# Performance work log

Measured on AMD Instinct MI355X. Metric: run time of the kernel, lower is better.

Reference implementation:

```python
import jax, jax.numpy as jnp
import numpy as np


def setup_inputs() -> dict:
    key = jax.random.key(0)
    k1, k2, k3, k4 = jax.random.split(key, 4)
    B, S, IN, OUT = 4, 2048, 4096, 16384
    x = jax.random.normal(k1, (B, S, IN), dtype=jnp.float32)
    # int8 quantized weights in [-127, 127]; stored as int8
    q_weight = jax.random.randint(k2, (OUT, IN), -127, 128, dtype=jnp.int32).astype(jnp.int8)
    scale = jax.random.uniform(k3, (1,), dtype=jnp.float32, minval=0.005, maxval=0.02)
    bias = jax.random.normal(k4, (OUT,), dtype=jnp.float32)
    return {"x": x, "q_weight": q_weight, "scale": scale, "bias": bias}


def reference(x, q_weight, scale, bias):
    # dequantize: int8 -> fp32, per-tensor scale, then cast to activation dtype
    w = (q_weight.astype(jnp.float32) * scale).astype(x.dtype)  # [OUT, IN]
    # F.linear: y = x @ w.T + bias
    return jnp.einsum('bsi,oi->bso', x, w) + bias.astype(x.dtype)
```

## Files before the change

kernel.cpp:

```cpp
#include <hip/hip_runtime.h>
#include <hip/hip_bf16.h>
#include <stdint.h>


typedef __attribute__((ext_vector_type(4))) float f32x4;
typedef __attribute__((ext_vector_type(4))) int i32x4;
typedef __attribute__((ext_vector_type(8))) short bf16x8s;
typedef __attribute__((ext_vector_type(4))) unsigned int u32x4;

__device__ __forceinline__ uint32_t f2bf_rne(float f) {
  uint32_t x = __float_as_uint(f);
  return (x + 0x7FFFu + ((x >> 16) & 1u)) >> 16;
}
__device__ __forceinline__ uint32_t pk2_rne(float lo, float hi) {
  return f2bf_rne(lo) | (f2bf_rne(hi) << 16);
}
__device__ __forceinline__ uint32_t pk2_trunc(float lo, float hi) {
  return (__float_as_uint(lo) >> 16) | (__float_as_uint(hi) & 0xFFFF0000u);
}

#define GLOAD_LDS16(g, l)                                        \
  __builtin_amdgcn_global_load_lds(                              \
      (const __attribute__((address_space(1))) void*)(g),        \
      (__attribute__((address_space(3))) void*)(l), 16, 0, 0)

__global__ __launch_bounds__(256) void quant_x_kernel(
    const float* __restrict__ x, int8_t* __restrict__ xq,
    float* __restrict__ rscale) {
  const int r = blockIdx.x;
  const int t = threadIdx.x;
  const f32x4* rp = (const f32x4*)(x + (size_t)r * 4096);
  f32x4 v[4];
#pragma unroll
  for (int j = 0; j < 4; ++j)
    v[j] = __builtin_nontemporal_load(rp + t + 256 * j);
  float m = 0.f;
#pragma unroll
  for (int j = 0; j < 4; ++j) {
    m = fmaxf(m, fabsf(v[j].x));
    m = fmaxf(m, fabsf(v[j].y));
    m = fmaxf(m, fabsf(v[j].z));
    m = fmaxf(m, fabsf(v[j].w));
  }
#pragma unroll
  for (int off = 32; off >= 1; off >>= 1)
    m = fmaxf(m, __shfl_xor(m, off, 64));
  __shared__ float wm[4];
  if ((t & 63) == 0) wm[t >> 6] = m;
  __syncthreads();
  float mm = fmaxf(fmaxf(wm[0], wm[1]), fmaxf(wm[2], wm[3]));
  mm = fmaxf(mm, 1e-20f);
  const float inv = 127.0f / mm;
  if (t == 0) rscale[r] = mm * (1.0f / 127.0f);
  uint32_t* orow = (uint32_t*)(xq + (size_t)r * 4096);
#pragma unroll
  for (int j = 0; j < 4; ++j) {
    int q0 = (int)rintf(v[j].x * inv);
    int q1 = (int)rintf(v[j].y * inv);
    int q2 = (int)rintf(v[j].z * inv);
    int q3 = (int)rintf(v[j].w * inv);
    q0 = max(-127, min(127, q0)); q1 = max(-127, min(127, q1));
    q2 = max(-127, min(127, q2)); q3 = max(-127, min(127, q3));
    uint32_t o = (uint32_t)(q0 & 0xFF) | ((uint32_t)(q1 & 0xFF) << 8) |
                 ((uint32_t)(q2 & 0xFF) << 16) | ((uint32_t)(q3 & 0xFF) << 24);
    orow[t + 256 * j] = o;
  }
}

__global__ __launch_bounds__(256) void conv_w_q_kernel(
    const int32_t* __restrict__ w, int8_t* __restrict__ wq, int n16) {
  const int stride = blockDim.x * gridDim.x;
  for (int i = blockIdx.x * blockDim.x + threadIdx.x; i < n16; i += stride) {
    u32x4 o;
#pragma unroll
    for (int j = 0; j < 4; ++j) {
      i32x4 a = __builtin_nontemporal_load((const i32x4*)w + i * 4 + j);
      uint32_t p = (uint32_t)(a.x & 0xFF) | ((uint32_t)(a.y & 0xFF) << 8) |
                   ((uint32_t)(a.z & 0xFF) << 16) |
                   ((uint32_t)(a.w & 0xFF) << 24);
      if (j == 0) o.x = p; else if (j == 1) o.y = p;
      else if (j == 2) o.z = p; else o.w = p;
    }
    ((u32x4*)wq)[i] = o;
  }
}


#define PIN() __builtin_amdgcn_sched_barrier(0)

#define BARRIER()                 \
  PIN();                          \
  __builtin_amdgcn_s_barrier();   \
  PIN()

#define WAIT4  asm volatile("s_waitcnt vmcnt(4)" ::: "memory"); PIN()
#define WAIT0  asm volatile("s_waitcnt vmcnt(0)" ::: "memory"); PIN()
#define WAITL0 asm volatile("s_waitcnt lgkmcnt(0)" ::: "memory"); PIN()
#define LG(N)  asm volatile("s_waitcnt lgkmcnt(" #N ")" ::: "memory"); PIN()

#define STAGE(mat_base, koffb, ldsbase)                                      \
  {                                                                          \
    GLOAD_LDS16((mat_base) + (size_t)srow * RSB + (koffb) + skch,            \
                (ldsbase) + tid * 16);                                       \
    GLOAD_LDS16((mat_base) + (size_t)(srow + 128) * RSB + (koffb) + skch,    \
                (ldsbase) + 8192 + tid * 16);                                \
  }

#define ABLK(buf, kk) ((buf) + (kk) * 16384)
#define BBLK(buf, kk) ((buf) + 32768 + (kk) * 16384)

#define DSR(dst, addr, OFF)                                                  \
  asm volatile("ds_read_b128 %0, %1 offset:" OFF : "=v"(dst) : "v"(addr))

#define READ12(da, db, blkoff)                                               \
  {                                                                          \
    uint32_t _aa = aoff + (blkoff), _bb = boff + (blkoff);                   \
    DSR(db[0], _bb, "0");    DSR(db[1], _bb, "1024");                        \
    DSR(db[2], _bb, "2048"); DSR(db[3], _bb, "3072");                        \
    DSR(da[0], _aa, "0");    DSR(da[1], _aa, "1024");                        \
    DSR(da[2], _aa, "2048"); DSR(da[3], _aa, "3072");                        \
    DSR(da[4], _aa, "4096"); DSR(da[5], _aa, "5120");                        \
    DSR(da[6], _aa, "6144"); DSR(da[7], _aa, "7168");                        \
  }

#define MFMA4(av, bv, j)                                                     \
  _Pragma("unroll") for (int ni = 0; ni < 4; ++ni)                           \
    acc[j][ni] = __builtin_amdgcn_mfma_i32_16x16x64_i8(                      \
        av[j], bv[ni], acc[j][ni], 0, 0, 0);

#define EPOCH_ILV(av, bv, xa, xb, blkoff)                                    \
  {                                                                          \
    uint32_t _aa = aoff + (blkoff), _bb = boff + (blkoff);                   \
    __builtin_amdgcn_s_setprio(1);                                           \
    DSR(xb[0], _bb, "0");    DSR(xb[1], _bb, "1024");   PIN();               \
    LG(9);  MFMA4(av, bv, 0);                           PIN();               \
    DSR(xb[2], _bb, "2048"); DSR(xb[3], _bb, "3072");   PIN();               \
    LG(10); MFMA4(av, bv, 1);                           PIN();               \
    DSR(xa[0], _aa, "0");    DSR(xa[1], _aa, "1024");   PIN();               \
    LG(11); MFMA4(av, bv, 2);                           PIN();               \
    DSR(xa[2], _aa, "2048"); DSR(xa[3], _aa, "3072");   PIN();               \
    LG(12); MFMA4(av, bv, 3);                           PIN();               \
    DSR(xa[4], _aa, "4096"); DSR(xa[5], _aa, "5120");   PIN();               \
    LG(13); MFMA4(av, bv, 4);                           PIN();               \
    DSR(xa[6], _aa, "6144"); DSR(xa[7], _aa, "7168");   PIN();               \
    LG(14); MFMA4(av, bv, 5);                           PIN();               \
    LG(13); MFMA4(av, bv, 6);                           PIN();               \
    LG(12); MFMA4(av, bv, 7);                                                \
    __builtin_amdgcn_s_setprio(0);                                           \
  }

#define MFMA32(av, bv)                                                       \
  __builtin_amdgcn_s_setprio(1);                                             \
  _Pragma("unroll") for (int j = 0; j < 8; ++j)                              \
    _Pragma("unroll") for (int ni = 0; ni < 4; ++ni)                         \
      acc[j][ni] = __builtin_amdgcn_mfma_i32_16x16x64_i8(                    \
          av[j], bv[ni], acc[j][ni], 0, 0, 0);                               \
  __builtin_amdgcn_s_setprio(0);

__global__ __launch_bounds__(512, 2) void qlinear_gemm_i8_kernel(
    const int8_t* __restrict__ Xq,
    const int8_t* __restrict__ Wq,
    const float* __restrict__ rscale,
    const float* __restrict__ scalep,
    const float* __restrict__ bias,
    float* __restrict__ Y)
{
  constexpr int N = 16384, K = 4096;
  constexpr int RSB = K;
  constexpr int NT = K / 128;

  extern __shared__ __align__(16) char lds[];

  const int tid  = threadIdx.x;
  const int lane = tid & 63;
  const int wid  = tid >> 6;
  const int wm   = wid >> 2;
  const int wn   = wid & 3;
  const int r16  = lane & 15;
  const int g4   = lane >> 4;
  const int chb  = (g4 ^ ((r16 >> 1) & 3)) << 4;

  const int srow = tid >> 2;
  const int skch = ((tid & 3) ^ ((tid >> 3) & 3)) * 16;

  const int bid = blockIdx.x;
  const int xcd = bid & 7;
  const int l   = bid >> 3;
  const int bm  = (xcd & 1) * 16 + (l >> 4);
  const int bn  = (xcd >> 1) * 16 + (l & 15);

  i32x4 acc[8][4];
#pragma unroll
  for (int i = 0; i < 8; ++i)
#pragma unroll
    for (int j = 0; j < 4; ++j) acc[i][j] = (i32x4)0;

  i32x4 pa[8], qa[8], pb[4], qb[4];

  const char* Xp = (const char*)Xq + (size_t)(bm * 256) * RSB;
  const char* Wp = (const char*)Wq + (size_t)(bn * 256) * RSB;

  const uint32_t ldsb = (uint32_t)(uintptr_t)(void*)lds;
  const uint32_t aoff = ldsb + (uint32_t)((wm * 128 + r16) * 64 + chb);
  const uint32_t boff = ldsb + (uint32_t)(32768 + (wn * 64 + r16) * 64 + chb);

  STAGE(Xp, 0,   ABLK(lds, 0));
  STAGE(Wp, 0,   BBLK(lds, 0));
  STAGE(Xp, 64,  ABLK(lds, 1));
  STAGE(Wp, 64,  BBLK(lds, 1));
  STAGE(Xp, 128, ABLK(lds + 65536, 0));
  STAGE(Wp, 128, BBLK(lds + 65536, 0));
  WAIT4;
  BARRIER();
  READ12(pa, pb, 0u);

  for (int t = 0; t <= NT - 3; ++t) {
    const uint32_t cur = (uint32_t)(t & 1) << 16;
    const uint32_t nxt = cur ^ 65536u;
    char* cb = lds + cur;
    char* nb = lds + nxt;
    const size_t k1n = (size_t)(t + 1) * 128;
    const size_t k2n = (size_t)(t + 2) * 128;
    STAGE(Xp, k1n + 64, ABLK(nb, 1));
    STAGE(Wp, k1n + 64, BBLK(nb, 1));
    EPOCH_ILV(pa, pb, qa, qb, cur + 16384u);
    WAIT4;
    BARRIER();
    STAGE(Xp, k2n, ABLK(cb, 0));
    STAGE(Wp, k2n, BBLK(cb, 0));
    EPOCH_ILV(qa, qb, pa, pb, nxt);
    WAIT4;
    BARRIER();
  }

  {
    const uint32_t cur = (uint32_t)((NT - 2) & 1) << 16;
    const uint32_t nxt = cur ^ 65536u;
    char* nb = lds + nxt;
    const size_t k1n = (size_t)(NT - 1) * 128;
    STAGE(Xp, k1n + 64, ABLK(nb, 1));
    STAGE(Wp, k1n + 64, BBLK(nb, 1));
    EPOCH_ILV(pa, pb, qa, qb, cur + 16384u);
    WAIT4;
    BARRIER();
    EPOCH_ILV(qa, qb, pa, pb, nxt);
    WAIT0;
    BARRIER();
    EPOCH_ILV(pa, pb, qa, qb, nxt + 16384u);
    WAITL0;
    MFMA32(qa, qb);
  }

  const float s = scalep[0];
  float bv[4];
#pragma unroll
  for (int ni = 0; ni < 4; ++ni)
    bv[ni] = bias[bn * 256 + wn * 64 + ni * 16 + r16];

#pragma unroll
  for (int mi = 0; mi < 8; ++mi) {
    const int grow0 = bm * 256 + wm * 128 + mi * 16 + g4 * 4;
#pragma unroll
    for (int r = 0; r < 4; ++r) {
      const float dr = s * rscale[grow0 + r];
      float* yp = Y + (size_t)(grow0 + r) * N + bn * 256 + wn * 64 + r16;
#pragma unroll
      for (int ni = 0; ni < 4; ++ni)
        yp[ni * 16] = (float)acc[mi][ni][r] * dr + bv[ni];
    }
  }
}

#define BM 128
#define BN 128
#define BK 64
#define LDKF (BK * 2)

__global__ __launch_bounds__(256, 2) void qlinear_fused_kernel(
    const float* __restrict__ X, const int32_t* __restrict__ W,
    const float* __restrict__ scalep, const float* __restrict__ bias,
    float* __restrict__ Y)
{
  constexpr int N = 16384, K = 4096;
  __shared__ __align__(16) char slds[(BM + BN) * LDKF];
  char* As = slds;
  char* Bs = slds + BM * LDKF;
  const int tid = threadIdx.x, lane = tid & 63, wid = tid >> 6;
  const int wr = wid >> 1, wc = wid & 1;
  const int nwg = gridDim.x, cpx = nwg >> 3, bid = blockIdx.x;
  const int swz = (bid & 7) * cpx + (bid >> 3);
  const int ntn = N / BN, bm = swz / ntn, bn = swz % ntn;
  const int r16 = lane & 15, g4 = lane >> 4;
  f32x4 acc[4][4];
#pragma unroll
  for (int i = 0; i < 4; ++i)
#pragma unroll
    for (int j = 0; j < 4; ++j) acc[i][j] = (f32x4)0.f;
  const float* Abase = X + (size_t)(bm * BM) * K;
  const int32_t* Bbase = W + (size_t)(bn * BN) * K;
  const int stg_col = (tid & 7) * 8;
  for (int kt = 0; kt < K / BK; ++kt) {
    const int kb = kt * BK;
    if (kt) __syncthreads();
#pragma unroll
    for (int i = 0; i < 4; ++i) {
      const int row = i * 32 + (tid >> 3);
      const float* p = Abase + (size_t)row * K + kb + stg_col;
      f32x4 v0 = *(const f32x4*)p;
      f32x4 v1 = *(const f32x4*)(p + 4);
      u32x4 o = {pk2_rne(v0.x, v0.y), pk2_rne(v0.z, v0.w),
                 pk2_rne(v1.x, v1.y), pk2_rne(v1.z, v1.w)};
      int byte = (row * LDKF + stg_col * 2) ^ ((row & 7) << 4);
      *(u32x4*)(As + byte) = o;
    }
#pragma unroll
    for (int i = 0; i < 4; ++i) {
      const int row = i * 32 + (tid >> 3);
      const int32_t* p = Bbase + (size_t)row * K + kb + stg_col;
      i32x4 v0 = *(const i32x4*)p;
      i32x4 v1 = *(const i32x4*)(p + 4);
      u32x4 o = {pk2_trunc((float)v0.x, (float)v0.y),
                 pk2_trunc((float)v0.z, (float)v0.w),
                 pk2_trunc((float)v1.x, (float)v1.y),
                 pk2_trunc((float)v1.z, (float)v1.w)};
      int byte = (row * LDKF + stg_col * 2) ^ ((row & 7) << 4);
      *(u32x4*)(Bs + byte) = o;
    }
    __syncthreads();
#pragma unroll
    for (int kk = 0; kk < 2; ++kk) {
      bf16x8s af[4], bfr[4];
#pragma unroll
      for (int mi = 0; mi < 4; ++mi) {
        const int row = wr * 64 + mi * 16 + r16;
        int byte = (row * LDKF + kk * 64 + g4 * 16) ^ ((row & 7) << 4);
        af[mi] = *(const bf16x8s*)(As + byte);
      }
#pragma unroll
      for (int ni = 0; ni < 4; ++ni) {
        const int row = wc * 64 + ni * 16 + r16;
        int byte = (row * LDKF + kk * 64 + g4 * 16) ^ ((row & 7) << 4);
        bfr[ni] = *(const bf16x8s*)(Bs + byte);
      }
#pragma unroll
      for (int mi = 0; mi < 4; ++mi)
#pragma unroll
        for (int ni = 0; ni < 4; ++ni)
          acc[mi][ni] = __builtin_amdgcn_mfma_f32_16x16x32_bf16(
              af[mi], bfr[ni], acc[mi][ni], 0, 0, 0);
    }
  }
  const float s = scalep[0];
  float bv[4];
#pragma unroll
  for (int ni = 0; ni < 4; ++ni)
    bv[ni] = bias[bn * BN + wc * 64 + ni * 16 + r16];
#pragma unroll
  for (int mi = 0; mi < 4; ++mi) {
    const int grow0 = bm * BM + wr * 64 + mi * 16 + g4 * 4;
#pragma unroll
    for (int r = 0; r < 4; ++r) {
      float* yp = Y + (size_t)(grow0 + r) * N + bn * BN + wc * 64 + r16;
#pragma unroll
      for (int ni = 0; ni < 4; ++ni)
        yp[ni * 16] = s * acc[mi][ni][r] + bv[ni];
    }
  }
}

extern "C" void kernel_launch(void* const* d_in, const int* in_sizes, int n_in,
                              void* d_out, int out_size, void* d_ws, size_t ws_size,
                              hipStream_t stream) {
  const float*   x  = (const float*)d_in[0];
  const int32_t* w  = (const int32_t*)d_in[1];
  const float*   sc = (const float*)d_in[2];
  const float*   bs = (const float*)d_in[3];
  float*         y  = (float*)d_out;

  constexpr size_t M = 8192, N = 16384, K = 4096;
  const size_t wq_bytes = N * K;
  const size_t xq_bytes = M * K;
  const size_t need = wq_bytes + xq_bytes + M * sizeof(float);

  if (ws_size >= need) {
    int8_t* wq = (int8_t*)d_ws;
    int8_t* xq = wq + wq_bytes;
    float*  rs = (float*)(xq + xq_bytes);
    hipFuncSetAttribute((const void*)qlinear_gemm_i8_kernel,
                        hipFuncAttributeMaxDynamicSharedMemorySize, 131072);
    quant_x_kernel<<<8192, 256, 0, stream>>>(x, xq, rs);
    conv_w_q_kernel<<<2048, 256, 0, stream>>>(w, wq, (int)(wq_bytes / 16));
    qlinear_gemm_i8_kernel<<<2048, 512, 131072, stream>>>(xq, wq, rs, sc, bs, y);
  } else {
    qlinear_fused_kernel<<<8192, 256, 0, stream>>>(x, w, sc, bs, y);
  }
}
```

Before: 615.4 us.

## Shrink int8 GEMM tile to 128x256 with 4 waves and simple double buffering

The int8 GEMM kernel moves from a 256x256 block tile with 8 waves and a deep interleaved prefetch pipeline to a 128x256 tile with 4 waves. It now uses a single K=64 step per iteration with a two-buffer LDS ping-pong of 48 KB, and launches twice as many blocks. The aims are lower LDS use and higher occupancy, plus simpler scheduling. In exchange it loses the register-level double buffering of LDS reads and waits for all outstanding global loads every iteration. The smaller M tile also lowers arithmetic intensity per byte loaded.

```diff
diff --git a/kernel.cpp b/kernel.cpp
--- a/kernel.cpp
+++ b/kernel.cpp
@@ -93,71 +93,63 @@
   __builtin_amdgcn_s_barrier();   \
   PIN()
 
-#define WAIT4  asm volatile("s_waitcnt vmcnt(4)" ::: "memory"); PIN()
-#define WAIT0  asm volatile("s_waitcnt vmcnt(0)" ::: "memory"); PIN()
-#define WAITL0 asm volatile("s_waitcnt lgkmcnt(0)" ::: "memory"); PIN()
-#define LG(N)  asm volatile("s_waitcnt lgkmcnt(" #N ")" ::: "memory"); PIN()
-
-#define STAGE(mat_base, koffb, ldsbase)                                      \
+#define WAIT0vm asm volatile("s_waitcnt vmcnt(0)" ::: "memory"); PIN()
+#define LG(N)   asm volatile("s_waitcnt lgkmcnt(" #N ")" ::: "memory"); PIN()
+
+#define STAGE_A(mat_base, koffb, ldsbase)                                    \
   {                                                                          \
     GLOAD_LDS16((mat_base) + (size_t)srow * RSB + (koffb) + skch,            \
                 (ldsbase) + tid * 16);                                       \
+    GLOAD_LDS16((mat_base) + (size_t)(srow + 64) * RSB + (koffb) + skch,     \
+                (ldsbase) + 4096 + tid * 16);                                \
+  }
+#define STAGE_B(mat_base, koffb, ldsbase)                                    \
+  {                                                                          \
+    GLOAD_LDS16((mat_base) + (size_t)srow * RSB + (koffb) + skch,            \
+                (ldsbase) + tid * 16);                                       \
+    GLOAD_LDS16((mat_base) + (size_t)(srow + 64) * RSB + (koffb) + skch,     \
+                (ldsbase) + 4096 + tid * 16);                                \
     GLOAD_LDS16((mat_base) + (size_t)(srow + 128) * RSB + (koffb) + skch,    \
                 (ldsbase) + 8192 + tid * 16);                                \
-  }
-
-#define ABLK(buf, kk) ((buf) + (kk) * 16384)
-#define BBLK(buf, kk) ((buf) + 32768 + (kk) * 16384)
+    GLOAD_LDS16((mat_base) + (size_t)(srow + 192) * RSB + (koffb) + skch,    \
+                (ldsbase) + 12288 + tid * 16);                               \
+  }
 
 #define DSR(dst, addr, OFF)                                                  \
   asm volatile("ds_read_b128 %0, %1 offset:" OFF : "=v"(dst) : "v"(addr))
 
-#define READ12(da, db, blkoff)                                               \
+#define READ12(da, db, bufoff)                                               \
   {                                                                          \
-    uint32_t _aa = aoff + (blkoff), _bb = boff + (blkoff);                   \
+    uint32_t _aa = aoff + (bufoff), _bb = boff + (bufoff);                   \
+    DSR(da[0], _aa, "0");    DSR(da[1], _aa, "1024");                        \
+    DSR(da[2], _aa, "2048"); DSR(da[3], _aa, "3072");                        \
     DSR(db[0], _bb, "0");    DSR(db[1], _bb, "1024");                        \
     DSR(db[2], _bb, "2048"); DSR(db[3], _bb, "3072");                        \
-    DSR(da[0], _aa, "0");    DSR(da[1], _aa, "1024");                        \
-    DSR(da[2], _aa, "2048"); DSR(da[3], _aa, "3072");                        \
-    DSR(da[4], _aa, "4096"); DSR(da[5], _aa, "5120");                        \
-    DSR(da[6], _aa, "6144"); DSR(da[7], _aa, "7168");                        \
-  }
-
-#define MFMA4(av, bv, j)                                                     \
-  _Pragma("unroll") for (int ni = 0; ni < 4; ++ni)                           \
-    acc[j][ni] = __builtin_amdgcn_mfma_i32_16x16x64_i8(                      \
-        av[j], bv[ni], acc[j][ni], 0, 0, 0);
-
-#define EPOCH_ILV(av, bv, xa, xb, blkoff)                                    \
+    DSR(db[4], _bb, "4096"); DSR(db[5], _bb, "5120");                        \
+    DSR(db[6], _bb, "6144"); DSR(db[7], _bb, "7168");                        \
+  }
+
+#define MFMA4C(da, db, ni)                                                   \
+  _Pragma("unroll") for (int mi = 0; mi < 4; ++mi)                           \
+    acc[mi][ni] = __builtin_amdgcn_mfma_i32_16x16x64_i8(                     \
+        da[mi], db[ni], acc[mi][ni], 0, 0, 0);
+
+#define COMPUTE(da, db, bufoff)                                              \
   {                                                                          \
-    uint32_t _aa = aoff + (blkoff), _bb = boff + (blkoff);                   \
+    READ12(da, db, bufoff);                                                  \
     __builtin_amdgcn_s_setprio(1);                                           \
-    DSR(xb[0], _bb, "0");    DSR(xb[1], _bb, "1024");   PIN();               \
-    LG(9);  MFMA4(av, bv, 0);                           PIN();               \
-    DSR(xb[2], _bb, "2048"); DSR(xb[3], _bb, "3072");   PIN();               \
-    LG(10); MFMA4(av, bv, 1);                           PIN();               \
-    DSR(xa[0], _aa, "0");    DSR(xa[1], _aa, "1024");   PIN();               \
-    LG(11); MFMA4(av, bv, 2);                           PIN();               \
-    DSR(xa[2], _aa, "2048"); DSR(xa[3], _aa, "3072");   PIN();               \
-    LG(12); MFMA4(av, bv, 3);                           PIN();               \
-    DSR(xa[4], _aa, "4096"); DSR(xa[5], _aa, "5120");   PIN();               \
-    LG(13); MFMA4(av, bv, 4);                           PIN();               \
-    DSR(xa[6], _aa, "6144"); DSR(xa[7], _aa, "7168");   PIN();               \
-    LG(14); MFMA4(av, bv, 5);                           PIN();               \
-    LG(13); MFMA4(av, bv, 6);                           PIN();               \
-    LG(12); MFMA4(av, bv, 7);                                                \
+    LG(7); MFMA4C(da, db, 0);   PIN();                                       \
+    LG(6); MFMA4C(da, db, 1);   PIN();                                       \
+    LG(5); MFMA4C(da, db, 2);   PIN();                                       \
+    LG(4); MFMA4C(da, db, 3);   PIN();                                       \
+    LG(3); MFMA4C(da, db, 4);   PIN();                                       \
+    LG(2); MFMA4C(da, db, 5);   PIN();                                       \
+    LG(1); MFMA4C(da, db, 6);   PIN();                                       \
+    LG(0); MFMA4C(da, db, 7);                                                \
     __builtin_amdgcn_s_setprio(0);                                           \
   }
 
-#define MFMA32(av, bv)                                                       \
-  __builtin_amdgcn_s_setprio(1);                                             \
-  _Pragma("unroll") for (int j = 0; j < 8; ++j)                              \
-    _Pragma("unroll") for (int ni = 0; ni < 4; ++ni)                         \
-      acc[j][ni] = __builtin_amdgcn_mfma_i32_16x16x64_i8(                    \
-          av[j], bv[ni], acc[j][ni], 0, 0, 0);                               \
-  __builtin_amdgcn_s_setprio(0);
-
-__global__ __launch_bounds__(512, 2) void qlinear_gemm_i8_kernel(
+__global__ __launch_bounds__(256, 2) void qlinear_gemm_i8_kernel(
     const int8_t* __restrict__ Xq,
     const int8_t* __restrict__ Wq,
     const float* __restrict__ rscale,
@@ -167,15 +159,15 @@
 {
   constexpr int N = 16384, K = 4096;
   constexpr int RSB = K;
-  constexpr int NT = K / 128;
+  constexpr int NT = K / 64;
 
   extern __shared__ __align__(16) char lds[];
 
   const int tid  = threadIdx.x;
   const int lane = tid & 63;
   const int wid  = tid >> 6;
-  const int wm   = wid >> 2;
-  const int wn   = wid & 3;
+  const int wm   = wid >> 1;
+  const int wn   = wid & 1;
   const int r16  = lane & 15;
   const int g4   = lane >> 4;
   const int chb  = (g4 ^ ((r16 >> 1) & 3)) << 4;
@@ -186,86 +178,59 @@
   const int bid = blockIdx.x;
   const int xcd = bid & 7;
   const int l   = bid >> 3;
-  const int bm  = (xcd & 1) * 16 + (l >> 4);
-  const int bn  = (xcd >> 1) * 16 + (l & 15);
-
-  i32x4 acc[8][4];
-#pragma unroll
-  for (int i = 0; i < 8; ++i)
-#pragma unroll
-    for (int j = 0; j < 4; ++j) acc[i][j] = (i32x4)0;
-
-  i32x4 pa[8], qa[8], pb[4], qb[4];
-
-  const char* Xp = (const char*)Xq + (size_t)(bm * 256) * RSB;
+  const int bm  = (xcd >> 1) * 16 + (l >> 5);
+  const int bn  = (xcd & 1) * 32 + (l & 31);
+
+  i32x4 acc[4][8];
+#pragma unroll
+  for (int i = 0; i < 4; ++i)
+#pragma unroll
+    for (int j = 0; j < 8; ++j) acc[i][j] = (i32x4)0;
+
+  i32x4 pa[4], pb[8];
+
+  const char* Xp = (const char*)Xq + (size_t)(bm * 128) * RSB;
   const char* Wp = (const char*)Wq + (size_t)(bn * 256) * RSB;
 
   const uint32_t ldsb = (uint32_t)(uintptr_t)(void*)lds;
-  const uint32_t aoff = ldsb + (uint32_t)((wm * 128 + r16) * 64 + chb);
-  const uint32_t boff = ldsb + (uint32_t)(32768 + (wn * 64 + r16) * 64 + chb);
-
-  STAGE(Xp, 0,   ABLK(lds, 0));
-  STAGE(Wp, 0,   BBLK(lds, 0));
-  STAGE(Xp, 64,  ABLK(lds, 1));
-  STAGE(Wp, 64,  BBLK(lds, 1));
-  STAGE(Xp, 128, ABLK(lds + 65536, 0));
-  STAGE(Wp, 128, BBLK(lds + 65536, 0));
-  WAIT4;
+  const uint32_t aoff = ldsb + (uint32_t)((wm * 64 + r16) * 64 + chb);
+  const uint32_t boff = ldsb + (uint32_t)(8192 + (wn * 128 + r16) * 64 + chb);
+
+  STAGE_A(Xp, 0, lds);
+  STAGE_B(Wp, 0, lds + 8192);
+  WAIT0vm;
   BARRIER();
-  READ12(pa, pb, 0u);
-
-  for (int t = 0; t <= NT - 3; ++t) {
-    const uint32_t cur = (uint32_t)(t & 1) << 16;
-    const uint32_t nxt = cur ^ 65536u;
-    char* cb = lds + cur;
-    char* nb = lds + nxt;
-    const size_t k1n = (size_t)(t + 1) * 128;
-    const size_t k2n = (size_t)(t + 2) * 128;
-    STAGE(Xp, k1n + 64, ABLK(nb, 1));
-    STAGE(Wp, k1n + 64, BBLK(nb, 1));
-    EPOCH_ILV(pa, pb, qa, qb, cur + 16384u);
-    WAIT4;
+
+  for (int u = 0; u <= NT - 2; ++u) {
+    const uint32_t cur = (uint32_t)(u & 1) * 24576u;
+    const uint32_t nxt = 24576u - cur;
+    const size_t kb = (size_t)(u + 1) * 64;
+    STAGE_A(Xp, kb, lds + nxt);
+    STAGE_B(Wp, kb, lds + nxt + 8192);
+    COMPUTE(pa, pb, cur);
+    WAIT0vm;
     BARRIER();
-    STAGE(Xp, k2n, ABLK(cb, 0));
-    STAGE(Wp, k2n, BBLK(cb, 0));
-    EPOCH_ILV(qa, qb, pa, pb, nxt);
-    WAIT4;
-    BARRIER();
-  }
-
+  }
   {
-    const uint32_t cur = (uint32_t)((NT - 2) & 1) << 16;
-    const uint32_t nxt = cur ^ 65536u;
-    char* nb = lds + nxt;
-    const size_t k1n = (size_t)(NT - 1) * 128;
-    STAGE(Xp, k1n + 64, ABLK(nb, 1));
-    STAGE(Wp, k1n + 64, BBLK(nb, 1));
-    EPOCH_ILV(pa, pb, qa, qb, cur + 16384u);
-    WAIT4;
-    BARRIER();
-    EPOCH_ILV(qa, qb, pa, pb, nxt);
-    WAIT0;
-    BARRIER();
-    EPOCH_ILV(pa, pb, qa, qb, nxt + 16384u);
-    WAITL0;
-    MFMA32(qa, qb);
+    const uint32_t cur = (uint32_t)((NT - 1) & 1) * 24576u;
+    COMPUTE(pa, pb, cur);
   }
 
   const float s = scalep[0];
-  float bv[4];
-#pragma unroll
-  for (int ni = 0; ni < 4; ++ni)
-    bv[ni] = bias[bn * 256 + wn * 64 + ni * 16 + r16];
-
-#pragma unroll
-  for (int mi = 0; mi < 8; ++mi) {
-    const int grow0 = bm * 256 + wm * 128 + mi * 16 + g4 * 4;
+  float bv[8];
+#pragma unroll
+  for (int ni = 0; ni < 8; ++ni)
+    bv[ni] = bias[bn * 256 + wn * 128 + ni * 16 + r16];
+
+#pragma unroll
+  for (int mi = 0; mi < 4; ++mi) {
+    const int grow0 = bm * 128 + wm * 64 + mi * 16 + g4 * 4;
 #pragma unroll
     for (int r = 0; r < 4; ++r) {
       const float dr = s * rscale[grow0 + r];
-      float* yp = Y + (size_t)(grow0 + r) * N + bn * 256 + wn * 64 + r16;
-#pragma unroll
-      for (int ni = 0; ni < 4; ++ni)
+      float* yp = Y + (size_t)(grow0 + r) * N + bn * 256 + wn * 128 + r16;
+#pragma unroll
+      for (int ni = 0; ni < 8; ++ni)
         yp[ni * 16] = (float)acc[mi][ni][r] * dr + bv[ni];
     }
   }
@@ -387,10 +352,10 @@
     int8_t* xq = wq + wq_bytes;
     float*  rs = (float*)(xq + xq_bytes);
     hipFuncSetAttribute((const void*)qlinear_gemm_i8_kernel,
-                        hipFuncAttributeMaxDynamicSharedMemorySize, 131072);
+                        hipFuncAttributeMaxDynamicSharedMemorySize, 49152);
     quant_x_kernel<<<8192, 256, 0, stream>>>(x, xq, rs);
     conv_w_q_kernel<<<2048, 256, 0, stream>>>(w, wq, (int)(wq_bytes / 16));
-    qlinear_gemm_i8_kernel<<<2048, 512, 131072, stream>>>(xq, wq, rs, sc, bs, y);
+    qlinear_gemm_i8_kernel<<<4096, 256, 49152, stream>>>(xq, wq, rs, sc, bs, y);
   } else {
     qlinear_fused_kernel<<<8192, 256, 0, stream>>>(x, w, sc, bs, y);
   }
```

Measured after the change: 732.5 us. 19.0% more time.
